# Performance work log

Measured on AMD Instinct MI355X. Metric: run time of the kernel, lower is better.

Reference implementation:

```python
import jax, jax.numpy as jnp
import numpy as np

EMBED_DIM = 768
N_HEADS = 12
HEAD_DIM = EMBED_DIM // N_HEADS


def setup_inputs() -> dict:
    key = jax.random.key(0)
    ks = jax.random.split(key, 6)
    bsz, seq = 2, 4096
    hidden_states = jax.random.normal(ks[0], (bsz, seq, EMBED_DIM), dtype=jnp.float32)
    attention_mask = jnp.zeros((bsz, 1, 1, seq), dtype=jnp.float32)
    s = 1.0 / np.sqrt(EMBED_DIM)
    Wq = jax.random.normal(ks[1], (EMBED_DIM, EMBED_DIM), dtype=jnp.float32) * s
    Wk = jax.random.normal(ks[2], (EMBED_DIM, EMBED_DIM), dtype=jnp.float32) * s
    Wv = jax.random.normal(ks[3], (EMBED_DIM, EMBED_DIM), dtype=jnp.float32) * s
    Wo = jax.random.normal(ks[4], (EMBED_DIM, EMBED_DIM), dtype=jnp.float32) * s
    bo = jax.random.normal(ks[5], (EMBED_DIM,), dtype=jnp.float32) * s
    return {"hidden_states": hidden_states, "attention_mask": attention_mask,
            "Wq": Wq, "Wk": Wk, "Wv": Wv, "Wo": Wo, "bo": bo}


def reference(hidden_states, attention_mask, Wq, Wk, Wv, Wo, bo):
    bsz, seq, _ = hidden_states.shape
    scale = 1.0 / np.sqrt(HEAD_DIM)

    def split_heads(x):  # [b, s, e] -> [b, h, s, d]
        return x.reshape(bsz, seq, N_HEADS, HEAD_DIM).transpose(0, 2, 1, 3)

    # nn.Linear applies x @ W.T
    q = split_heads(hidden_states @ Wq.T)
    k = split_heads(hidden_states @ Wk.T)
    v = split_heads(hidden_states @ Wv.T)

    # [b, h, tgt, src] score matrix (faithful to the bmm+softmax+bmm original)
    attn = jnp.einsum('bhqd,bhkd->bhqk', q, k) * scale
    attn = attn + attention_mask  # mask broadcasts [b,1,1,src]
    probs = jax.nn.softmax(attn, axis=-1)
    ctx = jnp.einsum('bhqk,bhkd->bhqd', probs, v)

    concat = ctx.transpose(0, 2, 1, 3).reshape(bsz, seq, EMBED_DIM)
    return concat @ Wo.T + bo
```

## Files before the change

### kernel.cpp

```cpp
#include <hip/hip_runtime.h>
#include <stdint.h>

#define ED   768
#define NH   12
#define HD   64
#define SEQ  4096
#define BSZ  2
#define BHT  (BSZ*NH)
#define MTOT (BSZ*SEQ)

typedef short bf16x8  __attribute__((ext_vector_type(8)));
typedef float f32x4   __attribute__((ext_vector_type(4)));
typedef float f32x16  __attribute__((ext_vector_type(16)));

#define LOG2E 1.44269504088896340736f
#define C2    (0.125f * LOG2E)

__device__ __forceinline__ unsigned short f2bf(float f) {
    union { float f; uint32_t u; } v; v.f = f;
    uint32_t u = v.u;
    u += 0x7fffu + ((u >> 16) & 1u);
    return (unsigned short)(u >> 16);
}

__device__ __forceinline__ void cp16(const unsigned short* g, unsigned short* l) {
    __builtin_amdgcn_global_load_lds(
        (const __attribute__((address_space(1))) unsigned int*)(const void*)g,
        (__attribute__((address_space(3))) unsigned int*)(void*)l,
        16, 0, 0);
}

#define H_CHUNKS  (MTOT * ED / 4)
#define W_CHUNKS  (ED * ED / 4)
#define CVT_TOTAL (H_CHUNKS + 4 * W_CHUNKS)

__global__ __launch_bounds__(256) void convert_bf16(
    const float* __restrict__ H,  const float* __restrict__ Wq,
    const float* __restrict__ Wk, const float* __restrict__ Wv,
    const float* __restrict__ Wo, unsigned short* __restrict__ dst,
    unsigned short* __restrict__ WoB) {
    int i4 = blockIdx.x * 256 + threadIdx.x;
    float4 v;
    ushort4* optr;
    if (i4 < H_CHUNKS) { v = ((const float4*)H)[i4]; optr = (ushort4*)dst + i4; }
    else {
        int j = i4 - H_CHUNKS;
        if (j < 3 * W_CHUNKS) {
            if (j < W_CHUNKS)          v = ((const float4*)Wq)[j];
            else if (j < 2 * W_CHUNKS) v = ((const float4*)Wk)[j - W_CHUNKS];
            else                       v = ((const float4*)Wv)[j - 2 * W_CHUNKS];
            optr = (ushort4*)dst + i4;
        } else {
            v = ((const float4*)Wo)[j - 3 * W_CHUNKS];
            optr = (ushort4*)WoB + (j - 3 * W_CHUNKS);
        }
    }
    ushort4 o;
    o.x = f2bf(v.x); o.y = f2bf(v.y); o.z = f2bf(v.z); o.w = f2bf(v.w);
    *optr = o;
}

__global__ __launch_bounds__(256) void qkv_gemm(
    const unsigned short* __restrict__ Hb,
    const unsigned short* __restrict__ Wb,
    unsigned short* __restrict__ qkv) {
    __shared__ __align__(16) unsigned short Ah[128 * 64];
    __shared__ __align__(16) unsigned short Bh[128 * 64];
    const int t = threadIdx.x, w = t >> 6, lane = t & 63;
    const int quad = lane >> 4, r16 = lane & 15;
    const int wm = w >> 1, wn = w & 1;
    const int m0 = blockIdx.y * 128, n0g = blockIdx.x * 128;
    const int wsel = n0g / ED, n0 = n0g % ED;
    const int lrow = lane >> 3;
    const int lchs = ((lane & 7) ^ (lrow & 7)) * 8;

    f32x4 acc[4][4] = {};
    for (int kt = 0; kt < ED / 64; ++kt) {
        const int k0 = kt * 64;
#pragma unroll
        for (int i = 0; i < 4; ++i) {
            int row = i * 32 + w * 8;
            cp16(&Hb[(size_t)(m0 + row + lrow) * ED + k0 + lchs], &Ah[row * 64]);
            cp16(&Wb[(size_t)(n0g + row + lrow) * ED + k0 + lchs], &Bh[row * 64]);
        }
        __syncthreads();
#pragma unroll
        for (int kk = 0; kk < 2; ++kk) {
            bf16x8 aF[4], bF[4];
#pragma unroll
            for (int mi = 0; mi < 4; ++mi) {
                int R = wm * 64 + mi * 16 + r16;
                aF[mi] = *(const bf16x8*)&Ah[R * 64 + (((kk * 4 + quad) ^ (r16 & 7)) * 8)];
            }
#pragma unroll
            for (int ni = 0; ni < 4; ++ni) {
                int R = wn * 64 + ni * 16 + r16;
                bF[ni] = *(const bf16x8*)&Bh[R * 64 + (((kk * 4 + quad) ^ (r16 & 7)) * 8)];
            }
            if (wsel == 2) {
#pragma unroll
                for (int mi = 0; mi < 4; ++mi)
#pragma unroll
                    for (int ni = 0; ni < 4; ++ni)
                        acc[mi][ni] = __builtin_amdgcn_mfma_f32_16x16x32_bf16(
                            bF[ni], aF[mi], acc[mi][ni], 0, 0, 0);
            } else {
#pragma unroll
                for (int mi = 0; mi < 4; ++mi)
#pragma unroll
                    for (int ni = 0; ni < 4; ++ni)
                        acc[mi][ni] = __builtin_amdgcn_mfma_f32_16x16x32_bf16(
                            aF[mi], bF[ni], acc[mi][ni], 0, 0, 0);
            }
        }
        __syncthreads();
    }
    const size_t WSZ = (size_t)BHT * SEQ * HD;
    if (wsel == 2) {
#pragma unroll
        for (int mi = 0; mi < 4; ++mi)
#pragma unroll
            for (int ni = 0; ni < 4; ++ni)
#pragma unroll
                for (int r = 0; r < 4; ++r) {
                    int m  = m0 + wm * 64 + mi * 16 + r16;
                    int nn = n0 + wn * 64 + ni * 16 + quad * 4 + r;
                    int b = m >> 12, s = m & 4095;
                    int hh = nn >> 6, dd = nn & 63;
                    qkv[2 * WSZ + (((size_t)b * NH + hh) * HD + dd) * SEQ + s] =
                        f2bf(acc[mi][ni][r]);
                }
    } else {
        const float sc = (wsel == 0) ? C2 : 1.0f;
#pragma unroll
        for (int mi = 0; mi < 4; ++mi)
#pragma unroll
            for (int ni = 0; ni < 4; ++ni)
#pragma unroll
                for (int r = 0; r < 4; ++r) {
                    int m = m0 + wm * 64 + mi * 16 + quad * 4 + r;
                    int b = m >> 12, s = m & 4095;
                    int nn = n0 + wn * 64 + ni * 16 + r16;
                    int hh = nn >> 6, dd = nn & 63;
                    size_t off = (((size_t)b * NH + hh) * SEQ + s) * HD + dd;
                    qkv[(size_t)wsel * WSZ + off] = f2bf(acc[mi][ni][r] * sc);
                }
    }
}

__global__ __launch_bounds__(256) void flash_attn(
    const unsigned short* __restrict__ qkv, const float* __restrict__ mask,
    unsigned short* __restrict__ ctx) {
    __shared__ __align__(16) unsigned short Ksm[64 * 64];
    __shared__ __align__(16) unsigned short Vtsm[64 * 64];
    __shared__ __align__(16) unsigned short Psm[4][32][72];
    __shared__ unsigned short Msm[64];
    const int t  = threadIdx.x;
    const int bh = blockIdx.y;
    const int b  = bh / NH;
    const int h  = bh % NH;
    const int qbase = blockIdx.x * 128;
    const size_t WSZ = (size_t)BHT * SEQ * HD;
    const unsigned short* Qp = qkv + (size_t)bh * SEQ * HD;
    const unsigned short* Kp = Qp + WSZ;
    const unsigned short* Vt = qkv + 2 * WSZ + (size_t)bh * HD * SEQ;
    const int w = t >> 6, lane = t & 63, n31 = lane & 31, hi = lane >> 5;
    const int lrow = lane >> 3;
    const int lchs = ((lane & 7) ^ (lrow & 7)) * 8;

    bf16x8 qF[4];
    {
        int qrow = qbase + w * 32 + n31;
#pragma unroll
        for (int kc = 0; kc < 4; ++kc)
            qF[kc] = *(const bf16x8*)&Qp[(size_t)qrow * HD + kc * 16 + hi * 8];
    }
    bf16x8 bOnes = {};
    if (hi == 0) bOnes[0] = (short)0x3F80;

    f32x16 oAcc[2] = {};
    float l_i = 0.0f;
    const int sw = n31 & 7;

    for (int kt = 0; kt < SEQ / 64; ++kt) {
#pragma unroll
        for (int i = 0; i < 2; ++i) {
            int row = w * 16 + i * 8;
            cp16(&Kp[(size_t)(kt * 64 + row + lrow) * HD + lchs], &Ksm[row * 64]);
            cp16(&Vt[(size_t)(row + lrow) * SEQ + kt * 64 + lchs], &Vtsm[row * 64]);
        }
        if (t < 64) Msm[t] = f2bf(LOG2E * mask[b * SEQ + kt * 64 + t]);
        __syncthreads();

        float p[2][16];
        float rs0 = 0.f, rs1 = 0.f, rs2 = 0.f, rs3 = 0.f;
#pragma unroll
        for (int st = 0; st < 2; ++st) {
            bf16x8 am = {};
            {
                unsigned short mv = Msm[st * 32 + n31];
                am[0] = (hi == 0) ? (short)mv : (short)0;
            }
            f32x16 sA = {};
            sA = __builtin_amdgcn_mfma_f32_32x32x16_bf16(am, bOnes, sA, 0, 0, 0);
#pragma unroll
            for (int kc = 0; kc < 4; ++kc) {
                bf16x8 kF = *(const bf16x8*)
                    &Ksm[(st * 32 + n31) * 64 + (((2 * kc + hi) ^ sw) * 8)];
                sA = __builtin_amdgcn_mfma_f32_32x32x16_bf16(kF, qF[kc], sA, 0, 0, 0);
            }
#pragma unroll
            for (int r = 0; r < 16; ++r) p[st][r] = __builtin_amdgcn_exp2f(sA[r]);
            rs0 += p[st][0] + p[st][4] + p[st][8]  + p[st][12];
            rs1 += p[st][1] + p[st][5] + p[st][9]  + p[st][13];
            rs2 += p[st][2] + p[st][6] + p[st][10] + p[st][14];
            rs3 += p[st][3] + p[st][7] + p[st][11] + p[st][15];
        }
        l_i += (rs0 + rs1) + (rs2 + rs3);

#pragma unroll
        for (int st = 0; st < 2; ++st)
#pragma unroll
            for (int g = 0; g < 4; ++g) {
                union { float f; uint32_t u; } a0, a1, a2, a3;
                a0.f = p[st][4 * g + 0]; a1.f = p[st][4 * g + 1];
                a2.f = p[st][4 * g + 2]; a3.f = p[st][4 * g + 3];
                uint32_t d0 = __builtin_amdgcn_perm(a1.u + 0x8000u, a0.u + 0x8000u, 0x07060302u);
                uint32_t d1 = __builtin_amdgcn_perm(a3.u + 0x8000u, a2.u + 0x8000u, 0x07060302u);
                uint2 dd; dd.x = d0; dd.y = d1;
                *(uint2*)&Psm[w][n31][st * 32 + hi * 4 + 8 * g] = dd;
            }

#pragma unroll
        for (int kc = 0; kc < 4; ++kc) {
            bf16x8 pF = *(const bf16x8*)&Psm[w][n31][kc * 16 + hi * 8];
#pragma unroll
            for (int dt = 0; dt < 2; ++dt) {
                bf16x8 vF = *(const bf16x8*)
                    &Vtsm[(dt * 32 + n31) * 64 + (((2 * kc + hi) ^ sw) * 8)];
                oAcc[dt] = __builtin_amdgcn_mfma_f32_32x32x16_bf16(vF, pF, oAcc[dt], 0, 0, 0);
            }
        }
        __syncthreads();
    }
    l_i += __shfl_xor(l_i, 32);
    float inv = 1.0f / l_i;
    int s = qbase + w * 32 + n31;
    unsigned short* obase = &ctx[((size_t)b * SEQ + s) * ED + h * HD];
#pragma unroll
    for (int dt = 0; dt < 2; ++dt)
#pragma unroll
        for (int g = 0; g < 4; ++g) {
            ushort4 o;
            o.x = f2bf(oAcc[dt][4 * g + 0] * inv);
            o.y = f2bf(oAcc[dt][4 * g + 1] * inv);
            o.z = f2bf(oAcc[dt][4 * g + 2] * inv);
            o.w = f2bf(oAcc[dt][4 * g + 3] * inv);
            *(ushort4*)&obase[dt * 32 + hi * 4 + 8 * g] = o;
        }
}

__global__ __launch_bounds__(256) void out_gemm(
    const unsigned short* __restrict__ Ab,
    const unsigned short* __restrict__ Wob,
    const float* __restrict__ bo, float* __restrict__ out) {
    __shared__ __align__(16) unsigned short Ah[128 * 64];
    __shared__ __align__(16) unsigned short Bh[128 * 64];
    const int t = threadIdx.x, w = t >> 6, lane = t & 63;
    const int quad = lane >> 4, r16 = lane & 15;
    const int wm = w >> 1, wn = w & 1;
    const int m0 = blockIdx.y * 128, n0 = blockIdx.x * 128;
    const int lrow = lane >> 3;
    const int lchs = ((lane & 7) ^ (lrow & 7)) * 8;

    f32x4 acc[4][4] = {};
    for (int kt = 0; kt < ED / 64; ++kt) {
        const int k0 = kt * 64;
#pragma unroll
        for (int i = 0; i < 4; ++i) {
            int row = i * 32 + w * 8;
            cp16(&Ab[(size_t)(m0 + row + lrow) * ED + k0 + lchs], &Ah[row * 64]);
            cp16(&Wob[(size_t)(n0 + row + lrow) * ED + k0 + lchs], &Bh[row * 64]);
        }
        __syncthreads();
#pragma unroll
        for (int kk = 0; kk < 2; ++kk) {
            bf16x8 aF[4], bF[4];
#pragma unroll
            for (int mi = 0; mi < 4; ++mi) {
                int R = wm * 64 + mi * 16 + r16;
                aF[mi] = *(const bf16x8*)&Ah[R * 64 + (((kk * 4 + quad) ^ (r16 & 7)) * 8)];
            }
#pragma unroll
            for (int ni = 0; ni < 4; ++ni) {
                int R = wn * 64 + ni * 16 + r16;
                bF[ni] = *(const bf16x8*)&Bh[R * 64 + (((kk * 4 + quad) ^ (r16 & 7)) * 8)];
            }
#pragma unroll
            for (int mi = 0; mi < 4; ++mi)
#pragma unroll
                for (int ni = 0; ni < 4; ++ni)
                    acc[mi][ni] = __builtin_amdgcn_mfma_f32_16x16x32_bf16(
                        aF[mi], bF[ni], acc[mi][ni], 0, 0, 0);
        }
        __syncthreads();
    }
    float bov[4];
#pragma unroll
    for (int ni = 0; ni < 4; ++ni) bov[ni] = bo[n0 + wn * 64 + ni * 16 + r16];
#pragma unroll
    for (int mi = 0; mi < 4; ++mi)
#pragma unroll
        for (int ni = 0; ni < 4; ++ni)
#pragma unroll
            for (int r = 0; r < 4; ++r) {
                int m = m0 + wm * 64 + mi * 16 + quad * 4 + r;
                int n = n0 + wn * 64 + ni * 16 + r16;
                out[(size_t)m * ED + n] = acc[mi][ni][r] + bov[ni];
            }
}

extern "C" void kernel_launch(void* const* d_in, const int* in_sizes, int n_in,
                              void* d_out, int out_size, void* d_ws, size_t ws_size,
                              hipStream_t stream) {
    const float* H    = (const float*)d_in[0];
    const float* mask = (const float*)d_in[1];
    const float* Wq   = (const float*)d_in[2];
    const float* Wk   = (const float*)d_in[3];
    const float* Wv   = (const float*)d_in[4];
    const float* Wo   = (const float*)d_in[5];
    const float* bo   = (const float*)d_in[6];
    unsigned short* ws = (unsigned short*)d_ws;
    const size_t WSZ = (size_t)BHT * SEQ * HD;
    unsigned short* qkv = ws;
    unsigned short* ctx = ws + 3 * WSZ;
    unsigned short* WoB = ctx + (size_t)MTOT * ED;
    float* out = (float*)d_out;
    unsigned short* Hb = (unsigned short*)d_out;
    unsigned short* Wb = Hb + (size_t)MTOT * ED;

    convert_bf16<<<CVT_TOTAL / 256, 256, 0, stream>>>(H, Wq, Wk, Wv, Wo, Hb, WoB);
    qkv_gemm<<<dim3(3 * ED / 128, MTOT / 128), 256, 0, stream>>>(Hb, Wb, qkv);
    flash_attn<<<dim3(SEQ / 128, BHT), 256, 0, stream>>>(qkv, mask, ctx);
    out_gemm<<<dim3(ED / 128, MTOT / 128), 256, 0, stream>>>(ctx, WoB, bo, out);
}
```

Measured before the change: 311.2 us.

## Double-buffer K/V tiles, preload mask, build P fragments in registers

K and V^T tiles are now double-buffered in LDS: the next tile is prefetched with global_load_lds while the current one is used, leaving one barrier per iteration instead of two. The whole mask row is converted to bf16 once at kernel start rather than once per tile. The P matrix is no longer round-tripped through LDS; it is packed with v_cvt_pk_bf16_f32 and rearranged across lanes with permlane32_swap to form the MFMA operand directly. s_setprio is raised around the MFMA blocks. LDS use grows (double buffers plus the full mask row), which may lower occupancy.

New measurement: 291.6 us. -6.3%, faster.

```diff
diff --git a/kernel.cpp b/kernel.cpp
--- a/kernel.cpp
+++ b/kernel.cpp
@@ -12,6 +12,7 @@
 typedef short bf16x8  __attribute__((ext_vector_type(8)));
 typedef float f32x4   __attribute__((ext_vector_type(4)));
 typedef float f32x16  __attribute__((ext_vector_type(16)));
+typedef unsigned int u32x4 __attribute__((ext_vector_type(4)));
 
 #define LOG2E 1.44269504088896340736f
 #define C2    (0.125f * LOG2E)
@@ -21,6 +22,12 @@
     uint32_t u = v.u;
     u += 0x7fffu + ((u >> 16) & 1u);
     return (unsigned short)(u >> 16);
+}
+
+__device__ __forceinline__ uint32_t cvtpk(float lo, float hi) {
+    uint32_t r;
+    asm("v_cvt_pk_bf16_f32 %0, %1, %2" : "=v"(r) : "v"(lo), "v"(hi));
+    return r;
 }
 
 __device__ __forceinline__ void cp16(const unsigned short* g, unsigned short* l) {
@@ -151,10 +158,9 @@
 __global__ __launch_bounds__(256) void flash_attn(
     const unsigned short* __restrict__ qkv, const float* __restrict__ mask,
     unsigned short* __restrict__ ctx) {
-    __shared__ __align__(16) unsigned short Ksm[64 * 64];
-    __shared__ __align__(16) unsigned short Vtsm[64 * 64];
-    __shared__ __align__(16) unsigned short Psm[4][32][72];
-    __shared__ unsigned short Msm[64];
+    __shared__ __align__(16) unsigned short Ksm[2][64 * 64];
+    __shared__ __align__(16) unsigned short Vtsm[2][64 * 64];
+    __shared__ __align__(16) unsigned short Mall[SEQ];
     const int t  = threadIdx.x;
     const int bh = blockIdx.y;
     const int b  = bh / NH;
@@ -178,19 +184,39 @@
     bf16x8 bOnes = {};
     if (hi == 0) bOnes[0] = (short)0x3F80;
 
+#pragma unroll
+    for (int i = 0; i < 4; ++i) {
+        float4 mv = ((const float4*)(mask + (size_t)b * SEQ))[i * 256 + t];
+        ushort4 o;
+        o.x = f2bf(LOG2E * mv.x); o.y = f2bf(LOG2E * mv.y);
+        o.z = f2bf(LOG2E * mv.z); o.w = f2bf(LOG2E * mv.w);
+        *(ushort4*)&Mall[(i * 256 + t) * 4] = o;
+    }
+
+#pragma unroll
+    for (int i = 0; i < 2; ++i) {
+        int row = w * 16 + i * 8;
+        cp16(&Kp[(size_t)(row + lrow) * HD + lchs], &Ksm[0][row * 64]);
+        cp16(&Vt[(size_t)(row + lrow) * SEQ + lchs], &Vtsm[0][row * 64]);
+    }
+    __syncthreads();
+
     f32x16 oAcc[2] = {};
     float l_i = 0.0f;
     const int sw = n31 & 7;
+    int cur = 0;
 
     for (int kt = 0; kt < SEQ / 64; ++kt) {
-#pragma unroll
-        for (int i = 0; i < 2; ++i) {
-            int row = w * 16 + i * 8;
-            cp16(&Kp[(size_t)(kt * 64 + row + lrow) * HD + lchs], &Ksm[row * 64]);
-            cp16(&Vt[(size_t)(row + lrow) * SEQ + kt * 64 + lchs], &Vtsm[row * 64]);
-        }
-        if (t < 64) Msm[t] = f2bf(LOG2E * mask[b * SEQ + kt * 64 + t]);
-        __syncthreads();
+        if (kt + 1 < SEQ / 64) {
+#pragma unroll
+            for (int i = 0; i < 2; ++i) {
+                int row = w * 16 + i * 8;
+                cp16(&Kp[(size_t)((kt + 1) * 64 + row + lrow) * HD + lchs],
+                     &Ksm[cur ^ 1][row * 64]);
+                cp16(&Vt[(size_t)(row + lrow) * SEQ + (kt + 1) * 64 + lchs],
+                     &Vtsm[cur ^ 1][row * 64]);
+            }
+        }
 
         float p[2][16];
         float rs0 = 0.f, rs1 = 0.f, rs2 = 0.f, rs3 = 0.f;
@@ -198,17 +224,19 @@
         for (int st = 0; st < 2; ++st) {
             bf16x8 am = {};
             {
-                unsigned short mv = Msm[st * 32 + n31];
+                unsigned short mv = Mall[kt * 64 + st * 32 + n31];
                 am[0] = (hi == 0) ? (short)mv : (short)0;
             }
             f32x16 sA = {};
             sA = __builtin_amdgcn_mfma_f32_32x32x16_bf16(am, bOnes, sA, 0, 0, 0);
+            __builtin_amdgcn_s_setprio(1);
 #pragma unroll
             for (int kc = 0; kc < 4; ++kc) {
                 bf16x8 kF = *(const bf16x8*)
-                    &Ksm[(st * 32 + n31) * 64 + (((2 * kc + hi) ^ sw) * 8)];
+                    &Ksm[cur][(st * 32 + n31) * 64 + (((2 * kc + hi) ^ sw) * 8)];
                 sA = __builtin_amdgcn_mfma_f32_32x32x16_bf16(kF, qF[kc], sA, 0, 0, 0);
             }
+            __builtin_amdgcn_s_setprio(0);
 #pragma unroll
             for (int r = 0; r < 16; ++r) p[st][r] = __builtin_amdgcn_exp2f(sA[r]);
             rs0 += p[st][0] + p[st][4] + p[st][8]  + p[st][12];
@@ -218,30 +246,39 @@
         }
         l_i += (rs0 + rs1) + (rs2 + rs3);
 
-#pragma unroll
-        for (int st = 0; st < 2; ++st)
-#pragma unroll
-            for (int g = 0; g < 4; ++g) {
-                union { float f; uint32_t u; } a0, a1, a2, a3;
-                a0.f = p[st][4 * g + 0]; a1.f = p[st][4 * g + 1];
-                a2.f = p[st][4 * g + 2]; a3.f = p[st][4 * g + 3];
-                uint32_t d0 = __builtin_amdgcn_perm(a1.u + 0x8000u, a0.u + 0x8000u, 0x07060302u);
-                uint32_t d1 = __builtin_amdgcn_perm(a3.u + 0x8000u, a2.u + 0x8000u, 0x07060302u);
-                uint2 dd; dd.x = d0; dd.y = d1;
-                *(uint2*)&Psm[w][n31][st * 32 + hi * 4 + 8 * g] = dd;
-            }
-
+        bf16x8 pF[4];
+#pragma unroll
+        for (int st = 0; st < 2; ++st) {
+            uint32_t pw[8];
+#pragma unroll
+            for (int i = 0; i < 8; ++i)
+                pw[i] = cvtpk(p[st][2 * i], p[st][2 * i + 1]);
+#pragma unroll
+            for (int half = 0; half < 2; ++half) {
+                auto r02 = __builtin_amdgcn_permlane32_swap(
+                    pw[half * 4 + 0], pw[half * 4 + 2], false, false);
+                auto r13 = __builtin_amdgcn_permlane32_swap(
+                    pw[half * 4 + 1], pw[half * 4 + 3], false, false);
+                union { u32x4 u; bf16x8 h; } f;
+                f.u[0] = r02[0]; f.u[1] = r13[0]; f.u[2] = r02[1]; f.u[3] = r13[1];
+                pF[st * 2 + half] = f.h;
+            }
+        }
+
+        __builtin_amdgcn_s_setprio(1);
 #pragma unroll
         for (int kc = 0; kc < 4; ++kc) {
-            bf16x8 pF = *(const bf16x8*)&Psm[w][n31][kc * 16 + hi * 8];
 #pragma unroll
             for (int dt = 0; dt < 2; ++dt) {
                 bf16x8 vF = *(const bf16x8*)
-                    &Vtsm[(dt * 32 + n31) * 64 + (((2 * kc + hi) ^ sw) * 8)];
-                oAcc[dt] = __builtin_amdgcn_mfma_f32_32x32x16_bf16(vF, pF, oAcc[dt], 0, 0, 0);
-            }
-        }
-        __syncthreads();
+                    &Vtsm[cur][(dt * 32 + n31) * 64 + (((2 * kc + hi) ^ sw) * 8)];
+                oAcc[dt] = __builtin_amdgcn_mfma_f32_32x32x16_bf16(vF, pF[kc], oAcc[dt], 0, 0, 0);
+            }
+        }
+        __builtin_amdgcn_s_setprio(0);
+
+        __syncthreads();
+        cur ^= 1;
     }
     l_i += __shfl_xor(l_i, 32);
     float inv = 1.0f / l_i;
```
